# Optimization experiments

Measured on AMD Instinct MI355X. Metric: run time of the kernel, lower is better.

Reference implementation:

```python
import jax, jax.numpy as jnp
import numpy as np

B, T, C = 4, 2048, 1024
H = 16
DH = C // H  # 64


def setup_inputs() -> dict:
    key = jax.random.key(0)
    ks = jax.random.split(key, 6)
    s = 1.0 / np.sqrt(C)
    x = jax.random.normal(ks[0], (B, T, C), dtype=jnp.float32)
    # per-head projection weights, stacked: (H, C, DH)
    Wq = jax.random.uniform(ks[1], (H, C, DH), dtype=jnp.float32, minval=-s, maxval=s)
    Wk = jax.random.uniform(ks[2], (H, C, DH), dtype=jnp.float32, minval=-s, maxval=s)
    Wv = jax.random.uniform(ks[3], (H, C, DH), dtype=jnp.float32, minval=-s, maxval=s)
    # output projection (torch Linear: y = x @ W.T + b); store as (C, C) for x @ Wo
    Wo = jax.random.uniform(ks[4], (C, C), dtype=jnp.float32, minval=-s, maxval=s)
    bo = jax.random.uniform(ks[5], (C,), dtype=jnp.float32, minval=-s, maxval=s)
    return {"x": x, "Wq": Wq, "Wk": Wk, "Wv": Wv, "Wo": Wo, "bo": bo}


def reference(x, Wq, Wk, Wv, Wo, bo):
    # x: (B,T,C) -> q,k,v: (B,H,T,DH)
    q = jnp.einsum('btc,hcd->bhtd', x, Wq)
    k = jnp.einsum('btc,hcd->bhtd', x, Wk)
    v = jnp.einsum('btc,hcd->bhtd', x, Wv)
    scale = DH ** -0.5
    scores = jnp.einsum('bhtd,bhsd->bhts', q, k) * scale  # (B,H,T,T)
    causal = jnp.tril(jnp.ones((T, T), dtype=bool))
    scores = jnp.where(causal, scores, -jnp.inf)
    wei = jax.nn.softmax(scores, axis=-1)
    out = jnp.einsum('bhts,bhsd->bhtd', wei, v)  # (B,H,T,DH)
    # concat heads: (B,T,H*DH) = (B,T,C)
    out = out.transpose(0, 2, 1, 3).reshape(B, T, C)
    return out @ Wo + bo
```

## Files before the change

kernel.cpp:

```cpp
#include <hip/hip_runtime.h>

#define T_SEQ 2048
#define C_DIM 1024
#define H_NUM 16
#define DHD   64
#define B_NUM 4
#define M_ROWS (B_NUM*T_SEQ)

typedef __bf16 bf16x8 __attribute__((ext_vector_type(8)));
typedef float  f32x4  __attribute__((ext_vector_type(4)));
typedef unsigned short ushort8 __attribute__((ext_vector_type(8)));
typedef unsigned short ushort4e __attribute__((ext_vector_type(4)));

__device__ __forceinline__ unsigned short f2b(float f){
  return __builtin_bit_cast(unsigned short, (__bf16)f);
}
__device__ __forceinline__ bf16x8 as_bf(ushort8 u){ return __builtin_bit_cast(bf16x8, u); }
__device__ __forceinline__ float exp2fast(float x){ return __builtin_amdgcn_exp2f(x); }

__device__ __forceinline__ void gload16(const void* g, void* l){
  __builtin_amdgcn_global_load_lds(
      (const __attribute__((address_space(1))) void*)g,
      (__attribute__((address_space(3))) void*)l, 16, 0, 0);
}

#define MF(a,b,c) __builtin_amdgcn_mfma_f32_16x16x32_bf16(a,b,c,0,0,0)

__global__ __launch_bounds__(256) void k_prep(const float* __restrict__ x,
                                              const float* __restrict__ wq,
                                              const float* __restrict__ wk,
                                              const float* __restrict__ wv,
                                              const float* __restrict__ wo,
                                              unsigned short* __restrict__ xb,
                                              unsigned short* __restrict__ wt,
                                              unsigned short* __restrict__ wot){
  const int bid = blockIdx.x;
  const int tid = threadIdx.x;
  if (bid < 8192){
    int i = bid*256 + tid;
    float4 f = ((const float4*)x)[i];
    ushort4e o;
    o[0]=f2b(f.x); o[1]=f2b(f.y); o[2]=f2b(f.z); o[3]=f2b(f.w);
    ((ushort4e*)xb)[i] = o;
    return;
  }
  __shared__ __align__(16) unsigned short vr[64][72];
  const int tb = bid - 8192;
  const float* S; int LS; unsigned short* D; int R0, C0; float scale = 1.f;
  if (tb < 768){
    int m = tb >> 8, rem = tb & 255;
    int h = rem >> 4, c0 = rem & 15;
    S = ((m==0)?wq:(m==1)?wk:wv) + (size_t)(h*16 + c0)*64*64;
    LS = 64;
    D = wt; R0 = m*1024 + h*64; C0 = c0*64;
    if (m == 0) scale = 0.125f * 1.4426950408889634f;
  } else {
    int tb2 = tb - 768;
    int nb = tb2 >> 4, cb = tb2 & 15;
    S = wo + (size_t)(cb*64)*1024 + nb*64;
    LS = 1024;
    D = wot; R0 = nb*64; C0 = cb*64;
  }
  #pragma unroll
  for (int i = 0; i < 2; i++){
    int id2 = tid + i*256;
    int r = id2 >> 3, e8 = (id2 & 7)*8;
    float4 a = *(const float4*)&S[(size_t)r*LS + e8];
    float4 b2 = *(const float4*)&S[(size_t)r*LS + e8 + 4];
    ushort8 u;
    u[0]=f2b(a.x*scale); u[1]=f2b(a.y*scale); u[2]=f2b(a.z*scale); u[3]=f2b(a.w*scale);
    u[4]=f2b(b2.x*scale); u[5]=f2b(b2.y*scale); u[6]=f2b(b2.z*scale); u[7]=f2b(b2.w*scale);
    *(ushort8*)&vr[r][e8 ^ ((r >> 3) << 3)] = u;
  }
  __syncthreads();
  #pragma unroll
  for (int i = 0; i < 2; i++){
    int id2 = tid + i*256;
    int d = id2 >> 3, oc = id2 & 7;
    ushort8 u;
    #pragma unroll
    for (int j = 0; j < 8; j++)
      u[j] = vr[oc*8 + j][d ^ (oc << 3)];
    *(ushort8*)&D[(size_t)(R0 + d)*1024 + C0 + oc*8] = u;
  }
}

__global__ __launch_bounds__(256) void k_gemm_qkv(const unsigned short* __restrict__ xb,
                                                  const unsigned short* __restrict__ wt,
                                                  unsigned short* __restrict__ qo,
                                                  unsigned short* __restrict__ ko,
                                                  unsigned short* __restrict__ vtr){
  __shared__ __align__(16) unsigned short smem[4][128*64];
  const int tid = threadIdx.x, lane = tid & 63, wid = tid >> 6;
  const int g = lane >> 4, tl = lane & 15;
  const int wr = wid >> 1, wc = wid & 1;
  const int id = blockIdx.x;
  const int xcd = id & 7, i = id >> 3;
  const int xm = xcd >> 1, xn = xcd & 1;
  const int mbase = (xm*16 + i/12) * 128, nbase = (xn*12 + i%12) * 128;
  const int sel = nbase >> 10;
  const int srow8 = lane >> 3, sj = lane & 7;
  f32x4 acc[4][4] = {};

#define QKV_STAGE(BUF, KK) do{                                                  \
    _Pragma("unroll")                                                           \
    for (int i2 = 0; i2 < 4; i2++){                                             \
      const int brow = (wid*4 + i2)*8;                                          \
      const int row  = brow + srow8;                                            \
      const int jj   = sj ^ (row & 7);                                          \
      gload16(&xb[(size_t)(mbase+row)*C_DIM + (KK) + jj*8], &smem[BUF][brow*64]);   \
      gload16(&wt[(size_t)(nbase+row)*C_DIM + (KK) + jj*8], &smem[2+(BUF)][brow*64]);\
    }                                                                           \
  }while(0)

#define QKV_FRAGS(BUF)                                                          \
    bf16x8 aF[4][2], bF[4][2];                                                  \
    _Pragma("unroll")                                                           \
    for (int mb = 0; mb < 4; mb++){                                             \
      const int row = wr*64 + mb*16 + tl; const int s7 = row & 7;               \
      aF[mb][0] = as_bf(*(const ushort8*)&smem[BUF][row*64 + ((g     ^ s7)*8)]);\
      aF[mb][1] = as_bf(*(const ushort8*)&smem[BUF][row*64 + (((4+g) ^ s7)*8)]);\
    }                                                                           \
    _Pragma("unroll")                                                           \
    for (int nb = 0; nb < 4; nb++){                                             \
      const int row = wc*64 + nb*16 + tl; const int s7 = row & 7;               \
      bF[nb][0] = as_bf(*(const ushort8*)&smem[2+(BUF)][row*64 + ((g     ^ s7)*8)]);\
      bF[nb][1] = as_bf(*(const ushort8*)&smem[2+(BUF)][row*64 + (((4+g) ^ s7)*8)]);\
    }

  if (sel < 2){
    QKV_STAGE(0, 0);
    __syncthreads();
    #pragma unroll 1
    for (int it = 0; it < 16; ++it){
      const int cur = it & 1;
      if (it + 1 < 16) QKV_STAGE(cur^1, (it+1)*64);
      QKV_FRAGS(cur);
      #pragma unroll
      for (int mb = 0; mb < 4; mb++)
        #pragma unroll
        for (int nb = 0; nb < 4; nb++){
          acc[mb][nb] = MF(bF[nb][0], aF[mb][0], acc[mb][nb]);
          acc[mb][nb] = MF(bF[nb][1], aF[mb][1], acc[mb][nb]);
        }
      __syncthreads();
    }
    unsigned short* dst0 = (sel == 0) ? qo : ko;
    const int nloc = (nbase & 1023) + wc*64;
    #pragma unroll
    for (int mb = 0; mb < 4; mb++){
      const int t = mbase + wr*64 + mb*16 + tl;
      const int b = t >> 11, tt = t & 2047;
      #pragma unroll
      for (int nb = 0; nb < 4; nb++){
        const int nw = nloc + nb*16 + g*4;
        const int h = nw >> 6, d0 = nw & 63;
        ushort4e pk;
        #pragma unroll
        for (int r = 0; r < 4; r++) pk[r] = f2b(acc[mb][nb][r]);
        *(ushort4e*)&dst0[(((size_t)(b*H_NUM + h))*T_SEQ + tt)*DHD + d0] = pk;
      }
    }
  } else {
    QKV_STAGE(0, 0);
    __syncthreads();
    #pragma unroll 1
    for (int it = 0; it < 16; ++it){
      const int cur = it & 1;
      if (it + 1 < 16) QKV_STAGE(cur^1, (it+1)*64);
      QKV_FRAGS(cur);
      #pragma unroll
      for (int mb = 0; mb < 4; mb++)
        #pragma unroll
        for (int nb = 0; nb < 4; nb++){
          acc[mb][nb] = MF(aF[mb][0], bF[nb][0], acc[mb][nb]);
          acc[mb][nb] = MF(aF[mb][1], bF[nb][1], acc[mb][nb]);
        }
      __syncthreads();
    }
    unsigned short* tr = &smem[0][0];
    #pragma unroll
    for (int mb = 0; mb < 4; mb++){
      #pragma unroll
      for (int nb = 0; nb < 4; nb++){
        const int n = wc*64 + nb*16 + tl;
        const int m0 = wr*64 + mb*16 + g*4;
        ushort4e pk;
        #pragma unroll
        for (int r = 0; r < 4; r++) pk[r] = f2b(acc[mb][nb][r]);
        *(ushort4e*)&tr[n*128 + (m0 ^ ((n & 15) << 3))] = pk;
      }
    }
    __syncthreads();
    const int hbase = (nbase - 2048) >> 6;
    const int b = mbase >> 11, tloc = mbase & 2047;
    const int n = tid >> 1, half = tid & 1;
    unsigned short* vdst = vtr + (((size_t)(b*H_NUM + hbase + (n >> 6)))*DHD + (n & 63))*T_SEQ
                           + tloc + half*64;
    const int nx = (n & 15) << 3;
    #pragma unroll
    for (int c8 = 0; c8 < 8; c8++){
      const int t0 = half*64 + (c8 >> 2)*32 + (c8 & 3)*4;
      ushort4e lo = *(const ushort4e*)&tr[n*128 + ((t0     ) ^ nx)];
      ushort4e hi = *(const ushort4e*)&tr[n*128 + ((t0 + 16) ^ nx)];
      ushort8 u;
      #pragma unroll
      for (int e = 0; e < 4; e++){ u[e] = lo[e]; u[4+e] = hi[e]; }
      *(ushort8*)&vdst[c8*8] = u;
    }
  }
#undef QKV_STAGE
#undef QKV_FRAGS
}

__global__ __launch_bounds__(512) void k_flash(const unsigned short* __restrict__ q,
                                               const unsigned short* __restrict__ k,
                                               const unsigned short* __restrict__ vtg,
                                               unsigned short* __restrict__ o){
  __shared__ __align__(16) unsigned short kbufs[2][256*64];
  __shared__ __align__(16) unsigned short vbufs[2][64*256];
  const int tid = threadIdx.x, lane = tid & 63, w = tid >> 6;
  const int g = lane >> 4, tl = lane & 15;
  const int id = blockIdx.x;
  const int swz = (id & 7)*32 + (id >> 3);
  const int bh = swz >> 2, bx = swz & 3;
  const int b = bh >> 4, h = bh & 15;
  const unsigned short* qb = q   + (size_t)bh * T_SEQ * DHD;
  const unsigned short* kb = k   + (size_t)bh * T_SEQ * DHD;
  const unsigned short* vb = vtg + (size_t)bh * (size_t)DHD * T_SEQ;
  const int lrow = lane >> 3, lj = lane & 7;
  const int s7 = tl & 7;
  const int vq = (lane >> 3) & 3;

  for (int pass = 0; pass < 2; ++pass){
    const int qt = pass ? (7 - bx) : bx;
    const int tbase = qt * 256;
    const int trow0 = tbase + w * 32;
    const int tmax = trow0 + 31;
    bf16x8 qF[2][2];
    #pragma unroll
    for (int tf = 0; tf < 2; tf++)
      #pragma unroll
      for (int ks = 0; ks < 2; ks++)
        qF[tf][ks] = as_bf(*(const ushort8*)&qb[(size_t)(trow0 + tf*16 + tl)*DHD + ks*32 + g*8]);
    f32x4 acc[2][4] = {};
    float mreg[2] = {-1e30f, -1e30f}, lreg[2] = {0.f, 0.f};
    const int nkt = qt + 1;
    #pragma unroll
    for (int i = 0; i < 4; i++){
      const int krow = i*64 + w*8 + lrow;
      gload16(&kb[(size_t)krow*DHD + ((lj ^ (krow & 7))*8)], &kbufs[0][(i*64 + w*8)*64]);
      const int vrow = i*16 + w*2 + (lane >> 5);
      gload16(&vb[(size_t)vrow*T_SEQ + vq*64 + ((lj ^ (vrow & 7))*8)], &vbufs[0][(i*16 + w*2)*256]);
    }
    __syncthreads();
    for (int kti = 0; kti < nkt; ++kti){
      const int cur = kti & 1;
      const int kb256 = kti * 256;
      if (kti + 1 < nkt){
        const int kb2 = kb256 + 256;
        #pragma unroll
        for (int i = 0; i < 4; i++){
          const int krow = i*64 + w*8 + lrow;
          gload16(&kb[(size_t)(kb2+krow)*DHD + ((lj ^ (krow & 7))*8)], &kbufs[cur^1][(i*64 + w*8)*64]);
          const int vrow = i*16 + w*2 + (lane >> 5);
          gload16(&vb[(size_t)vrow*T_SEQ + kb2 + vq*64 + ((lj ^ (vrow & 7))*8)], &vbufs[cur^1][(i*16 + w*2)*256]);
        }
      }
      #pragma unroll
      for (int sh = 0; sh < 2; sh++){
        const int kbase = kb256 + sh*128;
        if (kbase <= tmax){
          const unsigned short* kcur = &kbufs[cur][sh*128*64];
          const unsigned short* vcur = &vbufs[cur][0];
          f32x4 st[2][8] = {};
          __builtin_amdgcn_s_setprio(1);
          #pragma unroll
          for (int sf = 0; sf < 8; sf++){
            const int row = sf*16 + tl;
            const int r7 = row & 7;
            bf16x8 kf0 = as_bf(*(const ushort8*)&kcur[row*64 + ((g     ^ r7)*8)]);
            bf16x8 kf1 = as_bf(*(const ushort8*)&kcur[row*64 + (((4+g) ^ r7)*8)]);
            #pragma unroll
            for (int tf = 0; tf < 2; tf++){
              st[tf][sf] = MF(kf0, qF[tf][0], st[tf][sf]);
              st[tf][sf] = MF(kf1, qF[tf][1], st[tf][sf]);
            }
          }
          __builtin_amdgcn_s_setprio(0);
          if (kbase + 127 > trow0){
            #pragma unroll
            for (int tf = 0; tf < 2; tf++){
              int tg = trow0 + tf*16 + tl;
              #pragma unroll
              for (int sf = 0; sf < 8; sf++)
                #pragma unroll
                for (int r = 0; r < 4; r++)
                  if (kbase + sf*16 + g*4 + r > tg) st[tf][sf][r] = -1e30f;
            }
          }
          bf16x8 pa[2][4];
          #pragma unroll
          for (int tf = 0; tf < 2; tf++){
            float mloc = -1e30f;
            #pragma unroll
            for (int sf = 0; sf < 8; sf++)
              #pragma unroll
              for (int r = 0; r < 4; r++) mloc = fmaxf(mloc, st[tf][sf][r]);
            if (__any(mloc > mreg[tf] + 8.f)){
              float mrow = fmaxf(mloc, __shfl_xor(mloc, 16));
              mrow = fmaxf(mrow, __shfl_xor(mrow, 32));
              float mnew = fmaxf(mreg[tf], mrow);
              float alpha = exp2fast(mreg[tf] - mnew);
              mreg[tf] = mnew;
              lreg[tf] *= alpha;
              #pragma unroll
              for (int df = 0; df < 4; df++)
                #pragma unroll
                for (int r = 0; r < 4; r++) acc[tf][df][r] *= alpha;
            }
            float sum = 0.f;
            #pragma unroll
            for (int q4 = 0; q4 < 4; q4++){
              ushort8 uu;
              #pragma unroll
              for (int r = 0; r < 4; r++){
                float p0 = exp2fast(st[tf][2*q4  ][r] - mreg[tf]);
                float p1 = exp2fast(st[tf][2*q4+1][r] - mreg[tf]);
                sum += p0 + p1;
                uu[r]   = f2b(p0);
                uu[4+r] = f2b(p1);
              }
              pa[tf][q4] = as_bf(uu);
            }
            lreg[tf] += sum;
          }
          __builtin_amdgcn_s_setprio(1);
          #pragma unroll
          for (int df = 0; df < 4; df++){
            const int row = df*16 + tl;
            bf16x8 vfr[4];
            #pragma unroll
            for (int q4 = 0; q4 < 4; q4++)
              vfr[q4] = as_bf(*(const ushort8*)&vcur[row*256 + sh*128 + (q4 >> 1)*64 + (((4*(q4 & 1) + g) ^ s7)*8)]);
            #pragma unroll
            for (int tf = 0; tf < 2; tf++)
              #pragma unroll
              for (int q4 = 0; q4 < 4; q4++)
                acc[tf][df] = MF(vfr[q4], pa[tf][q4], acc[tf][df]);
          }
          __builtin_amdgcn_s_setprio(0);
        }
      }
      __syncthreads();
    }
    #pragma unroll
    for (int tf = 0; tf < 2; tf++){
      float l = lreg[tf];
      l += __shfl_xor(l, 16);
      l += __shfl_xor(l, 32);
      float inv = 1.f / l;
      int tg = trow0 + tf*16 + tl;
      #pragma unroll
      for (int df = 0; df < 4; df++){
        ushort4e ov;
        #pragma unroll
        for (int r = 0; r < 4; r++) ov[r] = f2b(acc[tf][df][r] * inv);
        *(ushort4e*)&o[((size_t)(b*T_SEQ + tg))*C_DIM + h*DHD + df*16 + g*4] = ov;
      }
    }
  }
}

__global__ __launch_bounds__(256) void k_gemm_proj(const unsigned short* __restrict__ ab,
                                                   const unsigned short* __restrict__ wot,
                                                   const float* __restrict__ bo,
                                                   float* __restrict__ out){
  __shared__ __align__(16) unsigned short a_lds[128*64];
  __shared__ __align__(16) unsigned short b_lds[128*64];
  const int tid = threadIdx.x, lane = tid & 63, wid = tid >> 6;
  const int g = lane >> 4, tl = lane & 15;
  const int wr = wid >> 1, wc = wid & 1;
  const int id = blockIdx.x;
  const int swz = (id & 7)*64 + (id >> 3);
  const int mbase = (swz >> 3) * 128, nbase = (swz & 7) * 128;
  f32x4 acc[4][4] = {};
  for (int kk = 0; kk < C_DIM; kk += 64){
    __syncthreads();
    #pragma unroll
    for (int i = 0; i < 4; i++){
      const int brow = (wid*4 + i)*8;
      const int row  = brow + (lane >> 3);
      const int jj   = (lane & 7) ^ (row & 7);
      gload16(&ab[(size_t)(mbase+row)*C_DIM + kk + jj*8],  &a_lds[brow*64]);
      gload16(&wot[(size_t)(nbase+row)*C_DIM + kk + jj*8], &b_lds[brow*64]);
    }
    __syncthreads();
    bf16x8 aF[4][2], bF[4][2];
    #pragma unroll
    for (int mb = 0; mb < 4; mb++){
      const int row = wr*64 + mb*16 + tl; const int s7 = row & 7;
      aF[mb][0] = as_bf(*(const ushort8*)&a_lds[row*64 + ((g     ^ s7)*8)]);
      aF[mb][1] = as_bf(*(const ushort8*)&a_lds[row*64 + (((4+g) ^ s7)*8)]);
    }
    #pragma unroll
    for (int nb = 0; nb < 4; nb++){
      const int row = wc*64 + nb*16 + tl; const int s7 = row & 7;
      bF[nb][0] = as_bf(*(const ushort8*)&b_lds[row*64 + ((g     ^ s7)*8)]);
      bF[nb][1] = as_bf(*(const ushort8*)&b_lds[row*64 + (((4+g) ^ s7)*8)]);
    }
    #pragma unroll
    for (int mb = 0; mb < 4; mb++)
      #pragma unroll
      for (int nb = 0; nb < 4; nb++){
        acc[mb][nb] = MF(aF[mb][0], bF[nb][0], acc[mb][nb]);
        acc[mb][nb] = MF(aF[mb][1], bF[nb][1], acc[mb][nb]);
      }
  }
  #pragma unroll
  for (int mb = 0; mb < 4; mb++){
    #pragma unroll
    for (int nb = 0; nb < 4; nb++){
      #pragma unroll
      for (int r = 0; r < 4; r++){
        int gr = mbase + wr*64 + mb*16 + g*4 + r;
        int gc = nbase + wc*64 + nb*16 + tl;
        out[(size_t)gr*C_DIM + gc] = acc[mb][nb][r] + bo[gc];
      }
    }
  }
}

extern "C" void kernel_launch(void* const* d_in, const int* in_sizes, int n_in,
                              void* d_out, int out_size, void* d_ws, size_t ws_size,
                              hipStream_t stream){
  const float* x  = (const float*)d_in[0];
  const float* Wq = (const float*)d_in[1];
  const float* Wk = (const float*)d_in[2];
  const float* Wv = (const float*)d_in[3];
  const float* Wo = (const float*)d_in[4];
  const float* bo = (const float*)d_in[5];
  float* out = (float*)d_out;

  char* p = (char*)d_ws;
  unsigned short* xb  = (unsigned short*)p; p += (size_t)M_ROWS*C_DIM*2;
  unsigned short* wt  = (unsigned short*)p; p += (size_t)3*C_DIM*C_DIM*2;
  unsigned short* wot = (unsigned short*)p; p += (size_t)C_DIM*C_DIM*2;
  unsigned short* Qb  = (unsigned short*)p; p += (size_t)M_ROWS*C_DIM*2;
  unsigned short* Kb  = (unsigned short*)p; p += (size_t)M_ROWS*C_DIM*2;
  unsigned short* Vtr = (unsigned short*)p; p += (size_t)M_ROWS*C_DIM*2;
  unsigned short* attn = xb;

  hipLaunchKernelGGL(k_prep, dim3(8192 + 1024), dim3(256), 0, stream,
                     x, Wq, Wk, Wv, Wo, xb, wt, wot);
  hipLaunchKernelGGL(k_gemm_qkv, dim3(1536), dim3(256), 0, stream,
                     xb, wt, Qb, Kb, Vtr);
  hipLaunchKernelGGL(k_flash, dim3(256), dim3(512), 0, stream,
                     Qb, Kb, Vtr, attn);
  hipLaunchKernelGGL(k_gemm_proj, dim3(512), dim3(256), 0, stream,
                     attn, wot, bo, out);
}
```

Measured before the change: 160.0 us.

## Split flash attention into one query tile per block and double-buffer projection GEMM

The flash kernel stops pairing two query tiles per block (a balanced pair processed in two passes). It now launches 512 blocks, each handling a single 256-row query tile, and reorders the block index so heavy and light tiles interleave across the grid. K/V staging tiles shrink from 256 to 128 keys, which halves LDS per block and may allow more blocks per CU. The output-projection GEMM gains double-buffered LDS staging, so the next K-slice load overlaps the current MFMA work and one barrier per iteration is dropped. The risks are load imbalance from the uneven causal work per block and more barrier iterations per key range.

```diff
diff --git a/kernel.cpp b/kernel.cpp
--- a/kernel.cpp
+++ b/kernel.cpp
@@ -217,157 +217,158 @@
                                                const unsigned short* __restrict__ k,
                                                const unsigned short* __restrict__ vtg,
                                                unsigned short* __restrict__ o){
-  __shared__ __align__(16) unsigned short kbufs[2][256*64];
-  __shared__ __align__(16) unsigned short vbufs[2][64*256];
+  __shared__ __align__(16) unsigned short kbufs[2][128*64];
+  __shared__ __align__(16) unsigned short vbufs[2][64*128];
   const int tid = threadIdx.x, lane = tid & 63, w = tid >> 6;
   const int g = lane >> 4, tl = lane & 15;
   const int id = blockIdx.x;
-  const int swz = (id & 7)*32 + (id >> 3);
-  const int bh = swz >> 2, bx = swz & 3;
+  const int kslot = id >> 3;
+  const int bh = (id & 7)*8 + (kslot & 7);
+  const int qsel = kslot >> 3;
+  const int qt = (qsel < 4) ? qsel : (11 - qsel);
   const int b = bh >> 4, h = bh & 15;
   const unsigned short* qb = q   + (size_t)bh * T_SEQ * DHD;
   const unsigned short* kb = k   + (size_t)bh * T_SEQ * DHD;
   const unsigned short* vb = vtg + (size_t)bh * (size_t)DHD * T_SEQ;
   const int lrow = lane >> 3, lj = lane & 7;
   const int s7 = tl & 7;
-  const int vq = (lane >> 3) & 3;
-
-  for (int pass = 0; pass < 2; ++pass){
-    const int qt = pass ? (7 - bx) : bx;
-    const int tbase = qt * 256;
-    const int trow0 = tbase + w * 32;
-    const int tmax = trow0 + 31;
-    bf16x8 qF[2][2];
-    #pragma unroll
-    for (int tf = 0; tf < 2; tf++)
-      #pragma unroll
-      for (int ks = 0; ks < 2; ks++)
-        qF[tf][ks] = as_bf(*(const ushort8*)&qb[(size_t)(trow0 + tf*16 + tl)*DHD + ks*32 + g*8]);
-    f32x4 acc[2][4] = {};
-    float mreg[2] = {-1e30f, -1e30f}, lreg[2] = {0.f, 0.f};
-    const int nkt = qt + 1;
-    #pragma unroll
-    for (int i = 0; i < 4; i++){
-      const int krow = i*64 + w*8 + lrow;
-      gload16(&kb[(size_t)krow*DHD + ((lj ^ (krow & 7))*8)], &kbufs[0][(i*64 + w*8)*64]);
-      const int vrow = i*16 + w*2 + (lane >> 5);
-      gload16(&vb[(size_t)vrow*T_SEQ + vq*64 + ((lj ^ (vrow & 7))*8)], &vbufs[0][(i*16 + w*2)*256]);
+  const int vre = lane >> 4;
+  const int vh  = (lane >> 3) & 1;
+  const int vcc = lane & 7;
+
+  const int tbase = qt * 256;
+  const int trow0 = tbase + w * 32;
+  const int tmax = trow0 + 31;
+  bf16x8 qF[2][2];
+  #pragma unroll
+  for (int tf = 0; tf < 2; tf++)
+    #pragma unroll
+    for (int ks = 0; ks < 2; ks++)
+      qF[tf][ks] = as_bf(*(const ushort8*)&qb[(size_t)(trow0 + tf*16 + tl)*DHD + ks*32 + g*8]);
+  f32x4 acc[2][4] = {};
+  float mreg[2] = {-1e30f, -1e30f}, lreg[2] = {0.f, 0.f};
+  const int nkt = 2*qt + 2;
+  #pragma unroll
+  for (int i = 0; i < 2; i++){
+    const int krow = i*64 + w*8 + lrow;
+    const int kjj  = lj ^ (krow & 7);
+    gload16(&kb[(size_t)krow*DHD + kjj*8], &kbufs[0][(i*64 + w*8)*64]);
+    const int vrow = i*32 + w*4 + vre;
+    const int vjj  = vcc ^ (vrow & 7);
+    gload16(&vb[(size_t)vrow*T_SEQ + vh*64 + vjj*8], &vbufs[0][(i*32 + w*4)*128]);
+  }
+  __syncthreads();
+  for (int kti = 0; kti < nkt; ++kti){
+    const int cur = kti & 1;
+    const int kbase = kti * 128;
+    if (kti + 1 < nkt){
+      const int kb2 = kbase + 128;
+      #pragma unroll
+      for (int i = 0; i < 2; i++){
+        const int krow = i*64 + w*8 + lrow;
+        const int kjj  = lj ^ (krow & 7);
+        gload16(&kb[(size_t)(kb2+krow)*DHD + kjj*8], &kbufs[cur^1][(i*64 + w*8)*64]);
+        const int vrow = i*32 + w*4 + vre;
+        const int vjj  = vcc ^ (vrow & 7);
+        gload16(&vb[(size_t)vrow*T_SEQ + kb2 + vh*64 + vjj*8], &vbufs[cur^1][(i*32 + w*4)*128]);
+      }
+    }
+    if (kbase <= tmax){
+      const unsigned short* kcur = kbufs[cur];
+      const unsigned short* vcur = vbufs[cur];
+      f32x4 st[2][8] = {};
+      __builtin_amdgcn_s_setprio(1);
+      #pragma unroll
+      for (int sf = 0; sf < 8; sf++){
+        const int row = sf*16 + tl;
+        const int r7 = row & 7;
+        bf16x8 kf0 = as_bf(*(const ushort8*)&kcur[row*64 + ((g     ^ r7)*8)]);
+        bf16x8 kf1 = as_bf(*(const ushort8*)&kcur[row*64 + (((4+g) ^ r7)*8)]);
+        #pragma unroll
+        for (int tf = 0; tf < 2; tf++){
+          st[tf][sf] = MF(kf0, qF[tf][0], st[tf][sf]);
+          st[tf][sf] = MF(kf1, qF[tf][1], st[tf][sf]);
+        }
+      }
+      __builtin_amdgcn_s_setprio(0);
+      if (kbase + 127 > trow0){
+        #pragma unroll
+        for (int tf = 0; tf < 2; tf++){
+          int tg = trow0 + tf*16 + tl;
+          #pragma unroll
+          for (int sf = 0; sf < 8; sf++)
+            #pragma unroll
+            for (int r = 0; r < 4; r++)
+              if (kbase + sf*16 + g*4 + r > tg) st[tf][sf][r] = -1e30f;
+        }
+      }
+      bf16x8 pa[2][4];
+      #pragma unroll
+      for (int tf = 0; tf < 2; tf++){
+        float mloc = -1e30f;
+        #pragma unroll
+        for (int sf = 0; sf < 8; sf++)
+          #pragma unroll
+          for (int r = 0; r < 4; r++) mloc = fmaxf(mloc, st[tf][sf][r]);
+        if (__any(mloc > mreg[tf] + 8.f)){
+          float mrow = fmaxf(mloc, __shfl_xor(mloc, 16));
+          mrow = fmaxf(mrow, __shfl_xor(mrow, 32));
+          float mnew = fmaxf(mreg[tf], mrow);
+          float alpha = exp2fast(mreg[tf] - mnew);
+          mreg[tf] = mnew;
+          lreg[tf] *= alpha;
+          #pragma unroll
+          for (int df = 0; df < 4; df++)
+            #pragma unroll
+            for (int r = 0; r < 4; r++) acc[tf][df][r] *= alpha;
+        }
+        float sum = 0.f;
+        #pragma unroll
+        for (int q4 = 0; q4 < 4; q4++){
+          ushort8 uu;
+          #pragma unroll
+          for (int r = 0; r < 4; r++){
+            float p0 = exp2fast(st[tf][2*q4  ][r] - mreg[tf]);
+            float p1 = exp2fast(st[tf][2*q4+1][r] - mreg[tf]);
+            sum += p0 + p1;
+            uu[r]   = f2b(p0);
+            uu[4+r] = f2b(p1);
+          }
+          pa[tf][q4] = as_bf(uu);
+        }
+        lreg[tf] += sum;
+      }
+      __builtin_amdgcn_s_setprio(1);
+      #pragma unroll
+      for (int df = 0; df < 4; df++){
+        const int row = df*16 + tl;
+        bf16x8 vfr[4];
+        #pragma unroll
+        for (int q4 = 0; q4 < 4; q4++)
+          vfr[q4] = as_bf(*(const ushort8*)&vcur[row*128 + (q4 >> 1)*64 + (((4*(q4 & 1) + g) ^ s7)*8)]);
+        #pragma unroll
+        for (int tf = 0; tf < 2; tf++)
+          #pragma unroll
+          for (int q4 = 0; q4 < 4; q4++)
+            acc[tf][df] = MF(vfr[q4], pa[tf][q4], acc[tf][df]);
+      }
+      __builtin_amdgcn_s_setprio(0);
     }
     __syncthreads();
-    for (int kti = 0; kti < nkt; ++kti){
-      const int cur = kti & 1;
-      const int kb256 = kti * 256;
-      if (kti + 1 < nkt){
-        const int kb2 = kb256 + 256;
-        #pragma unroll
-        for (int i = 0; i < 4; i++){
-          const int krow = i*64 + w*8 + lrow;
-          gload16(&kb[(size_t)(kb2+krow)*DHD + ((lj ^ (krow & 7))*8)], &kbufs[cur^1][(i*64 + w*8)*64]);
-          const int vrow = i*16 + w*2 + (lane >> 5);
-          gload16(&vb[(size_t)vrow*T_SEQ + kb2 + vq*64 + ((lj ^ (vrow & 7))*8)], &vbufs[cur^1][(i*16 + w*2)*256]);
-        }
-      }
-      #pragma unroll
-      for (int sh = 0; sh < 2; sh++){
-        const int kbase = kb256 + sh*128;
-        if (kbase <= tmax){
-          const unsigned short* kcur = &kbufs[cur][sh*128*64];
-          const unsigned short* vcur = &vbufs[cur][0];
-          f32x4 st[2][8] = {};
-          __builtin_amdgcn_s_setprio(1);
-          #pragma unroll
-          for (int sf = 0; sf < 8; sf++){
-            const int row = sf*16 + tl;
-            const int r7 = row & 7;
-            bf16x8 kf0 = as_bf(*(const ushort8*)&kcur[row*64 + ((g     ^ r7)*8)]);
-            bf16x8 kf1 = as_bf(*(const ushort8*)&kcur[row*64 + (((4+g) ^ r7)*8)]);
-            #pragma unroll
-            for (int tf = 0; tf < 2; tf++){
-              st[tf][sf] = MF(kf0, qF[tf][0], st[tf][sf]);
-              st[tf][sf] = MF(kf1, qF[tf][1], st[tf][sf]);
-            }
-          }
-          __builtin_amdgcn_s_setprio(0);
-          if (kbase + 127 > trow0){
-            #pragma unroll
-            for (int tf = 0; tf < 2; tf++){
-              int tg = trow0 + tf*16 + tl;
-              #pragma unroll
-              for (int sf = 0; sf < 8; sf++)
-                #pragma unroll
-                for (int r = 0; r < 4; r++)
-                  if (kbase + sf*16 + g*4 + r > tg) st[tf][sf][r] = -1e30f;
-            }
-          }
-          bf16x8 pa[2][4];
-          #pragma unroll
-          for (int tf = 0; tf < 2; tf++){
-            float mloc = -1e30f;
-            #pragma unroll
-            for (int sf = 0; sf < 8; sf++)
-              #pragma unroll
-              for (int r = 0; r < 4; r++) mloc = fmaxf(mloc, st[tf][sf][r]);
-            if (__any(mloc > mreg[tf] + 8.f)){
-              float mrow = fmaxf(mloc, __shfl_xor(mloc, 16));
-              mrow = fmaxf(mrow, __shfl_xor(mrow, 32));
-              float mnew = fmaxf(mreg[tf], mrow);
-              float alpha = exp2fast(mreg[tf] - mnew);
-              mreg[tf] = mnew;
-              lreg[tf] *= alpha;
-              #pragma unroll
-              for (int df = 0; df < 4; df++)
-                #pragma unroll
-                for (int r = 0; r < 4; r++) acc[tf][df][r] *= alpha;
-            }
-            float sum = 0.f;
-            #pragma unroll
-            for (int q4 = 0; q4 < 4; q4++){
-              ushort8 uu;
-              #pragma unroll
-              for (int r = 0; r < 4; r++){
-                float p0 = exp2fast(st[tf][2*q4  ][r] - mreg[tf]);
-                float p1 = exp2fast(st[tf][2*q4+1][r] - mreg[tf]);
-                sum += p0 + p1;
-                uu[r]   = f2b(p0);
-                uu[4+r] = f2b(p1);
-              }
-              pa[tf][q4] = as_bf(uu);
-            }
-            lreg[tf] += sum;
-          }
-          __builtin_amdgcn_s_setprio(1);
-          #pragma unroll
-          for (int df = 0; df < 4; df++){
-            const int row = df*16 + tl;
-            bf16x8 vfr[4];
-            #pragma unroll
-            for (int q4 = 0; q4 < 4; q4++)
-              vfr[q4] = as_bf(*(const ushort8*)&vcur[row*256 + sh*128 + (q4 >> 1)*64 + (((4*(q4 & 1) + g) ^ s7)*8)]);
-            #pragma unroll
-            for (int tf = 0; tf < 2; tf++)
-              #pragma unroll
-              for (int q4 = 0; q4 < 4; q4++)
-                acc[tf][df] = MF(vfr[q4], pa[tf][q4], acc[tf][df]);
-          }
-          __builtin_amdgcn_s_setprio(0);
-        }
-      }
-      __syncthreads();
-    }
-    #pragma unroll
-    for (int tf = 0; tf < 2; tf++){
-      float l = lreg[tf];
-      l += __shfl_xor(l, 16);
-      l += __shfl_xor(l, 32);
-      float inv = 1.f / l;
-      int tg = trow0 + tf*16 + tl;
-      #pragma unroll
-      for (int df = 0; df < 4; df++){
-        ushort4e ov;
-        #pragma unroll
-        for (int r = 0; r < 4; r++) ov[r] = f2b(acc[tf][df][r] * inv);
-        *(ushort4e*)&o[((size_t)(b*T_SEQ + tg))*C_DIM + h*DHD + df*16 + g*4] = ov;
-      }
+  }
+  #pragma unroll
+  for (int tf = 0; tf < 2; tf++){
+    float l = lreg[tf];
+    l += __shfl_xor(l, 16);
+    l += __shfl_xor(l, 32);
+    float inv = 1.f / l;
+    int tg = trow0 + tf*16 + tl;
+    #pragma unroll
+    for (int df = 0; df < 4; df++){
+      ushort4e ov;
+      #pragma unroll
+      for (int r = 0; r < 4; r++) ov[r] = f2b(acc[tf][df][r] * inv);
+      *(ushort4e*)&o[((size_t)(b*T_SEQ + tg))*C_DIM + h*DHD + df*16 + g*4] = ov;
     }
   }
 }
@@ -376,38 +377,45 @@
                                                    const unsigned short* __restrict__ wot,
                                                    const float* __restrict__ bo,
                                                    float* __restrict__ out){
-  __shared__ __align__(16) unsigned short a_lds[128*64];
-  __shared__ __align__(16) unsigned short b_lds[128*64];
+  __shared__ __align__(16) unsigned short smem[4][128*64];
   const int tid = threadIdx.x, lane = tid & 63, wid = tid >> 6;
   const int g = lane >> 4, tl = lane & 15;
   const int wr = wid >> 1, wc = wid & 1;
   const int id = blockIdx.x;
   const int swz = (id & 7)*64 + (id >> 3);
   const int mbase = (swz >> 3) * 128, nbase = (swz & 7) * 128;
+  const int srow8 = lane >> 3, sj = lane & 7;
   f32x4 acc[4][4] = {};
-  for (int kk = 0; kk < C_DIM; kk += 64){
-    __syncthreads();
-    #pragma unroll
-    for (int i = 0; i < 4; i++){
-      const int brow = (wid*4 + i)*8;
-      const int row  = brow + (lane >> 3);
-      const int jj   = (lane & 7) ^ (row & 7);
-      gload16(&ab[(size_t)(mbase+row)*C_DIM + kk + jj*8],  &a_lds[brow*64]);
-      gload16(&wot[(size_t)(nbase+row)*C_DIM + kk + jj*8], &b_lds[brow*64]);
-    }
-    __syncthreads();
+
+#define PJ_STAGE(BUF, KK) do{                                                   \
+    _Pragma("unroll")                                                           \
+    for (int i2 = 0; i2 < 4; i2++){                                             \
+      const int brow = (wid*4 + i2)*8;                                          \
+      const int row  = brow + srow8;                                            \
+      const int jj   = sj ^ (row & 7);                                          \
+      gload16(&ab[(size_t)(mbase+row)*C_DIM + (KK) + jj*8],  &smem[BUF][brow*64]);   \
+      gload16(&wot[(size_t)(nbase+row)*C_DIM + (KK) + jj*8], &smem[2+(BUF)][brow*64]);\
+    }                                                                           \
+  }while(0)
+
+  PJ_STAGE(0, 0);
+  __syncthreads();
+  #pragma unroll 1
+  for (int it = 0; it < 16; ++it){
+    const int cur = it & 1;
+    if (it + 1 < 16) PJ_STAGE(cur^1, (it+1)*64);
     bf16x8 aF[4][2], bF[4][2];
     #pragma unroll
     for (int mb = 0; mb < 4; mb++){
       const int row = wr*64 + mb*16 + tl; const int s7 = row & 7;
-      aF[mb][0] = as_bf(*(const ushort8*)&a_lds[row*64 + ((g     ^ s7)*8)]);
-      aF[mb][1] = as_bf(*(const ushort8*)&a_lds[row*64 + (((4+g) ^ s7)*8)]);
+      aF[mb][0] = as_bf(*(const ushort8*)&smem[cur][row*64 + ((g     ^ s7)*8)]);
+      aF[mb][1] = as_bf(*(const ushort8*)&smem[cur][row*64 + (((4+g) ^ s7)*8)]);
     }
     #pragma unroll
     for (int nb = 0; nb < 4; nb++){
       const int row = wc*64 + nb*16 + tl; const int s7 = row & 7;
-      bF[nb][0] = as_bf(*(const ushort8*)&b_lds[row*64 + ((g     ^ s7)*8)]);
-      bF[nb][1] = as_bf(*(const ushort8*)&b_lds[row*64 + (((4+g) ^ s7)*8)]);
+      bF[nb][0] = as_bf(*(const ushort8*)&smem[2+cur][row*64 + ((g     ^ s7)*8)]);
+      bF[nb][1] = as_bf(*(const ushort8*)&smem[2+cur][row*64 + (((4+g) ^ s7)*8)]);
     }
     #pragma unroll
     for (int mb = 0; mb < 4; mb++)
@@ -416,7 +424,9 @@
         acc[mb][nb] = MF(aF[mb][0], bF[nb][0], acc[mb][nb]);
         acc[mb][nb] = MF(aF[mb][1], bF[nb][1], acc[mb][nb]);
       }
-  }
+    __syncthreads();
+  }
+#undef PJ_STAGE
   #pragma unroll
   for (int mb = 0; mb < 4; mb++){
     #pragma unroll
@@ -455,7 +465,7 @@
                      x, Wq, Wk, Wv, Wo, xb, wt, wot);
   hipLaunchKernelGGL(k_gemm_qkv, dim3(1536), dim3(256), 0, stream,
                      xb, wt, Qb, Kb, Vtr);
-  hipLaunchKernelGGL(k_flash, dim3(256), dim3(512), 0, stream,
+  hipLaunchKernelGGL(k_flash, dim3(512), dim3(512), 0, stream,
                      Qb, Kb, Vtr, attn);
   hipLaunchKernelGGL(k_gemm_proj, dim3(512), dim3(256), 0, stream,
                      attn, wot, bo, out);
```

Measured after the change: 156.9 us. About the same (-1.9%).
